# Performance work log

Measured on AMD Instinct MI355X. Metric: run time of the kernel, lower is better.

The kernel has to match this reference:

```python
import jax, jax.numpy as jnp
import numpy as np

N_FFT = 512
HOP = 160
N_ITER = 32
PAD = N_FFT // 2
TWO_PI = 2.0 * np.pi


def _stft(x, window):
    # x: [B, L] real -> spec [B, T, F] complex, center=True reflect pad (torch.stft)
    xp = jnp.pad(x, ((0, 0), (PAD, PAD)), mode='reflect')
    T = 1 + (xp.shape[-1] - N_FFT) // HOP
    idx = jnp.arange(T)[:, None] * HOP + jnp.arange(N_FFT)[None, :]  # [T, n_fft]
    frames = xp[:, idx] * window  # [B, T, n_fft]
    return jnp.fft.rfft(frames, axis=-1)  # [B, T, F]


def _istft(spec, window):
    # spec: [B, T, F] complex -> waveform [B, (T-1)*HOP] (torch.istft, center=True, length=None)
    frames = jnp.fft.irfft(spec, n=N_FFT, axis=-1) * window  # [B, T, n_fft]
    B, T, _ = frames.shape
    out_len = N_FFT + HOP * (T - 1)
    idx = (jnp.arange(T)[:, None] * HOP + jnp.arange(N_FFT)[None, :]).reshape(-1)
    y = jnp.zeros((B, out_len), frames.dtype).at[:, idx].add(frames.reshape(B, -1))
    wsq = jnp.zeros((out_len,), window.dtype).at[idx].add(jnp.tile(window * window, T))
    y = y / jnp.where(wsq > 1e-11, wsq, 1.0)  # NOLA normalization
    return y[:, PAD:out_len - PAD]


def setup_inputs() -> dict:
    key = jax.random.key(0)
    k1, k2 = jax.random.split(key)
    magnitude = jax.random.uniform(k1, (32, 1024, 257), dtype=jnp.float32)
    angles_init = jax.random.normal(k2, (32, 1024, 257), dtype=jnp.float32) * TWO_PI
    # hann window, periodic (torch.hann_window default)
    window = (0.5 * (1.0 - jnp.cos(TWO_PI * jnp.arange(N_FFT) / N_FFT))).astype(jnp.float32)
    return {"magnitude": magnitude, "angles_init": angles_init, "window": window}


def reference(magnitude, angles_init, window):
    # magnitude: [B, T, F]. Internally we keep [B, T, F] layout (torch transposes to
    # [B, F, T] before stft/istft; the math is identical, only the layout differs).
    mag = magnitude

    def step(angles, _):
        spec = mag * (jnp.cos(angles) + 1j * jnp.sin(angles))  # mag * exp(i*angles)
        wav = _istft(spec, window)
        rec = _stft(wav, window)
        new_angles = jnp.arctan2(rec.imag, rec.real)  # torch.angle
        return new_angles, None

    angles, _ = jax.lax.scan(step, angles_init, None, length=N_ITER)
    final_spec = mag * (jnp.cos(angles) + 1j * jnp.sin(angles))
    return _istft(final_spec, window)  # [B, (T-1)*HOP] = [32, 163680]
```

## Files before the change

kernel.cpp:

```cpp
#include <hip/hip_runtime.h>
#include <math.h>

#define BATCH 32
#define TFRAMES 1024
#define NBINS 257
#define NFFT 512
#define HOP 160
#define LOUT 163680
#define XPLEN 164192
#define NITER 32
#define FPW 4
#define WSTRIDE (FPW*HOP)
#define BSTRIDE (2*WSTRIDE)
#define HALO (NFFT-HOP)
#define WSPAN (WSTRIDE+HALO)
#define SPAN (BSTRIDE+HALO)
#define NBLK 128
#define SLOT SPAN
#define SB ((size_t)NBLK*SLOT)
#define SBUF ((size_t)BATCH*SB)

#define P2(i) ((i) + ((i) >> 4))

__device__ __forceinline__ float cosr(float x){ return __builtin_amdgcn_cosf(x); }
__device__ __forceinline__ float sinr(float x){ return __builtin_amdgcn_sinf(x); }
__device__ __forceinline__ void wsync(){
    __builtin_amdgcn_fence(__ATOMIC_SEQ_CST, "wavefront");
    __builtin_amdgcn_wave_barrier();
}
__device__ __forceinline__ float bperm(int addr, float v){
    return __int_as_float(__builtin_amdgcn_ds_bpermute(addr, __float_as_int(v)));
}

struct Tw { float c1,s1,c2,s2,c3,s3; };
__device__ __forceinline__ Tw twset(float x){
    Tw t; float c=cosr(x), s=sinr(x);
    t.c1=c; t.s1=s;
    t.c2=c*c-s*s; t.s2=2.f*c*s;
    t.c3=t.c2*c-t.s2*s; t.s3=t.c2*s+t.s2*c;
    return t;
}

template<int SIGN, bool TWID>
__device__ __forceinline__ void bfly4(const float xr[4], const float xi[4],
                                      const Tw& t, float yr[4], float yi[4]){
    constexpr float SG = (SIGN>0)?1.f:-1.f;
    float apc_r=xr[0]+xr[2], apc_i=xi[0]+xi[2];
    float amc_r=xr[0]-xr[2], amc_i=xi[0]-xi[2];
    float bpd_r=xr[1]+xr[3], bpd_i=xi[1]+xi[3];
    float bmd_r=xr[1]-xr[3], bmd_i=xi[1]-xi[3];
    yr[0]=apc_r+bpd_r; yi[0]=apc_i+bpd_i;
    float u2r=apc_r-bpd_r, u2i=apc_i-bpd_i;
    float u1r=amc_r-SG*bmd_i, u1i=amc_i+SG*bmd_r;
    float u3r=amc_r+SG*bmd_i, u3i=amc_i-SG*bmd_r;
    if (TWID){
        float s1=SG*t.s1, s2=SG*t.s2, s3=SG*t.s3;
        yr[1]=t.c1*u1r-s1*u1i; yi[1]=t.c1*u1i+s1*u1r;
        yr[2]=t.c2*u2r-s2*u2i; yi[2]=t.c2*u2i+s2*u2r;
        yr[3]=t.c3*u3r-s3*u3i; yi[3]=t.c3*u3i+s3*u3r;
    } else {
        yr[1]=u1r; yi[1]=u1i; yr[2]=u2r; yi[2]=u2i; yr[3]=u3r; yi[3]=u3i;
    }
}

template<int SIGN>
__device__ __forceinline__ void fft256reg(float xr[4], float xi[4],
                                          float2* __restrict__ bz,
                                          const Tw& tw0, const Tw& tw1, const Tw& tw2,
                                          int lane){
    float yr[4], yi[4], ar[4], ai[4];
    bfly4<SIGN,true>(xr, xi, tw0, yr, yi);
    { int o = 4*lane;
#pragma unroll
      for (int c=0;c<4;++c) bz[P2(o+c)] = make_float2(yr[c], yi[c]); }
    wsync();
#pragma unroll
    for (int c=0;c<4;++c){ float2 v = bz[P2(lane+64*c)]; ar[c]=v.x; ai[c]=v.y; }
    wsync();
    bfly4<SIGN,true>(ar, ai, tw1, yr, yi);
    { int o = (lane&3) + 16*(lane>>2);
#pragma unroll
      for (int c=0;c<4;++c) bz[P2(o+4*c)] = make_float2(yr[c], yi[c]); }
    wsync();
#pragma unroll
    for (int c=0;c<4;++c){ float2 v = bz[P2(lane+64*c)]; ar[c]=v.x; ai[c]=v.y; }
    wsync();
    bfly4<SIGN,true>(ar, ai, tw2, yr, yi);
    { int o = (lane&15) + 64*(lane>>4);
#pragma unroll
      for (int c=0;c<4;++c) bz[P2(o+16*c)] = make_float2(yr[c], yi[c]); }
    wsync();
#pragma unroll
    for (int c=0;c<4;++c){ float2 v = bz[P2(lane+64*c)]; ar[c]=v.x; ai[c]=v.y; }
    wsync();
    bfly4<SIGN,false>(ar, ai, tw0, xr, xi);
}

__global__ __launch_bounds__(256) void k_init(const float* __restrict__ win,
                                              float* __restrict__ wsqi){
    int i = blockIdx.x*256 + threadIdx.x;
    if (i < XPLEN){
        int n = i;
        int tmax = n / HOP; if (tmax > TFRAMES-1) tmax = TFRAMES-1;
        int tmin = (n - (NFFT-1) + (HOP-1)) / HOP; if (tmin < 0) tmin = 0;
        float acc = 0.f;
        for (int t = tmin; t <= tmax; ++t){ float w = win[n - t*HOP]; acc += w*w; }
        wsqi[i] = 1.0f / (acc > 1e-11f ? acc : 1.0f);
    }
}

__device__ __forceinline__ float xs(const float* __restrict__ Sb,
                                    const float* __restrict__ wsq, int p){
    int bxp = p / BSTRIDE, r = p - bxp*BSTRIDE;
    float a = 0.f;
    if (bxp < NBLK) a = Sb[(size_t)bxp*SLOT + r];
    if (r < HALO && bxp > 0) a += Sb[(size_t)(bxp-1)*SLOT + BSTRIDE + r];
    return a * wsq[p];
}
__device__ __forceinline__ float2 xs2(const float* __restrict__ Sb,
                                      const float* __restrict__ wsq, int p){
    int bxp = p / BSTRIDE, r = p - bxp*BSTRIDE;
    float2 acc = make_float2(0.f, 0.f);
    if (bxp < NBLK) acc = *(const float2*)(Sb + (size_t)bxp*SLOT + r);
    if (r < HALO && bxp > 0){
        float2 h = *(const float2*)(Sb + (size_t)(bxp-1)*SLOT + BSTRIDE + r);
        acc.x += h.x; acc.y += h.y;
    }
    float2 q = *(const float2*)(wsq + p);
    return make_float2(acc.x*q.x, acc.y*q.y);
}

__device__ __forceinline__ void inv_accum(float pr[4], float pi[4],
                                          float2* __restrict__ bz,
                                          const Tw& tw0, const Tw& tw1, const Tw& tw2,
                                          const float wA[4], const float wB[4],
                                          int lane, int f, float2* sa2){
    fft256reg<+1>(pr, pi, bz, tw0, tw1, tw2, lane);
    constexpr float SC = 1.f/256.f;
    int base2 = f*(HOP/2);
#pragma unroll
    for (int c=0;c<4;++c){
        int u = base2 + lane + 64*c;
        float2 v = sa2[u];
        v.x += pr[c]*wA[c]*SC;
        v.y += pi[c]*wB[c]*SC;
        sa2[u] = v;
    }
    wsync();
}

__device__ __forceinline__ void slot_store(float* __restrict__ Sw, int b, int bx,
                                           const float* s0, const float* s1, int tid){
    float2* slot2 = (float2*)(Sw + ((size_t)b*NBLK + bx)*SLOT);
    const float2* s0_2 = (const float2*)s0;
    const float2* s1_2 = (const float2*)s1;
#pragma unroll
    for (int j=0;j<7;++j){
        int u = tid + 128*j;
        if (u < SPAN/2){
            float2 v = make_float2(0.f, 0.f);
            if (u < WSPAN/2) v = s0_2[u];
            if (u >= WSTRIDE/2){
                float2 w1 = s1_2[u - WSTRIDE/2];
                v.x += w1.x; v.y += w1.y;
            }
            slot2[u] = v;
        }
    }
}

__device__ __forceinline__ void load_frame(const float* __restrict__ Sb,
                                           const float* __restrict__ wsq,
                                           int t, int lane,
                                           const float wA[4], const float wB[4],
                                           float fr[4], float fi[4]){
    bool edge = (t < 2) | (t >= TFRAMES-2);
    if (!edge){
        int pb = t*HOP;
#pragma unroll
        for (int c=0;c<4;++c){
            int p = pb + 2*(lane + 64*c);
            float2 v = xs2(Sb, wsq, p);
            fr[c] = v.x*wA[c];
            fi[c] = v.y*wB[c];
        }
    } else {
#pragma unroll
        for (int c=0;c<4;++c){
            int m = lane + 64*c;
            int p0 = t*HOP + 2*m, p1 = p0+1;
            int n0 = (p0<256)?(512-p0):((p0>=LOUT+256)?(2*LOUT+510-p0):p0);
            int n1 = (p1<256)?(512-p1):((p1>=LOUT+256)?(2*LOUT+510-p1):p1);
            fr[c] = xs(Sb, wsq, n0)*wA[c];
            fi[c] = xs(Sb, wsq, n1)*wB[c];
        }
    }
}

__device__ __forceinline__ void spectral(const float fr[4], const float fi[4],
                                         const float yr[4], const float yi[4],
                                         const float* __restrict__ magp,
                                         const float twc[4], const float tws[4],
                                         int lane, float pr[4], float pi[4]){
#pragma unroll
    for (int c=0;c<4;++c){
        int k = lane + 64*c;
        float zr = fr[c], zi = fi[c];
        float Xer = 0.5f*(zr+yr[c]), Xei = 0.5f*(zi-yi[c]);
        float Dr = zr-yr[c], Di = zi+yi[c];
        float Xor = 0.5f*Di, Xoi = -0.5f*Dr;
        float Or = twc[c]*Xor + tws[c]*Xoi;
        float Oi = twc[c]*Xoi - tws[c]*Xor;
        float X1r = Xer + Or, X1i = Xei + Oi;
        float X2r = Xer - Or, X2i = Oi - Xei;
        float q1 = X1r*X1r + X1i*X1i;
        bool ok1 = q1 > 1e-30f;
        float v1 = ok1 ? __builtin_amdgcn_rsqf(q1) : 0.f;
        float c1 = ok1 ? X1r*v1 : 1.f, s1 = X1i*v1;
        float q2 = X2r*X2r + X2i*X2i;
        bool ok2 = q2 > 1e-30f;
        float v2 = ok2 ? __builtin_amdgcn_rsqf(q2) : 0.f;
        float c2 = ok2 ? X2r*v2 : 1.f, s2 = X2i*v2;
        float m1 = magp[k], m2 = magp[256-k];
        float S1r = m1*c1, S1i = m1*s1;
        float S2r = m2*c2, S2i = m2*s2;
        float Aer = 0.5f*(S1r+S2r), Aei = 0.5f*(S1i-S2i);
        float Er = S1r - S2r, Ei = S1i + S2i;
        float Bor = 0.5f*(twc[c]*Er - tws[c]*Ei);
        float Boi = 0.5f*(twc[c]*Ei + tws[c]*Er);
        pr[c] = Aer - Boi;
        pi[c] = Aei + Bor;
    }
}

__global__ __launch_bounds__(128,4) void k_gl(const float* __restrict__ Sr,
                                              float* __restrict__ Sw,
                                              const float* __restrict__ mag,
                                              const float* __restrict__ win,
                                              const float* __restrict__ wsq){
    __shared__ __align__(16) float sacc[2][WSPAN];
    __shared__ __align__(16) float2 BZ[2][274];
    int tid = threadIdx.x, w = tid>>6, lane = tid&63;
    int b = blockIdx.y, bx = blockIdx.x;

    float2* bz = BZ[w];
    float2* sa2 = (float2*)sacc[w];

    Tw tw0 = twset((float)lane * (1.f/256.f));
    Tw tw1 = twset((float)(lane>>2) * (1.f/64.f));
    Tw tw2 = twset((float)(lane>>4) * (1.f/16.f));
    float twc[4], tws[4], wA[4], wB[4];
#pragma unroll
    for (int c=0;c<4;++c){
        int k = lane + 64*c;
        float x = (float)k * (1.f/512.f);
        twc[c]=cosr(x); tws[c]=sinr(x);
        float2 wv = ((const float2*)win)[k];
        wA[c]=wv.x; wB[c]=wv.y;
    }
    int am = ((64 - lane) & 63) << 2;
    bool l0 = (lane == 0);
#pragma unroll
    for (int j=0;j<8;++j){ int u = lane + 64*j; if (u < WSPAN/2) sa2[u]=make_float2(0.f,0.f); }
    __syncthreads();

    const float* Sb = Sr + (size_t)b*SB;
    const float* magb = mag + ((size_t)b*TFRAMES)*NBINS;
    int t0 = (bx*2 + w)*FPW;

#pragma unroll 1
    for (int f=0; f<FPW; ++f){
        int t = t0 + f;
        float fr[4], fi[4];
        load_frame(Sb, wsq, t, lane, wA, wB, fr, fi);

        fft256reg<-1>(fr, fi, bz, tw0, tw1, tw2, lane);

        float yr[4], yi[4];
#pragma unroll
        for (int c=0;c<4;++c){
            float gr = bperm(am, fr[3-c]);
            float gi = bperm(am, fi[3-c]);
            yr[c] = l0 ? fr[(4-c)&3] : gr;
            yi[c] = l0 ? fi[(4-c)&3] : gi;
        }

        float pr[4], pi[4];
        spectral(fr, fi, yr, yi, magb + (size_t)t*NBINS, twc, tws, lane, pr, pi);

        inv_accum(pr, pi, bz, tw0, tw1, tw2, wA, wB, lane, f, sa2);
    }
    __syncthreads();
    slot_store(Sw, b, bx, sacc[0], sacc[1], tid);
}

__global__ __launch_bounds__(128,4) void k_inv0s(const float* __restrict__ mag,
                                                 const float* __restrict__ ang,
                                                 const float* __restrict__ win,
                                                 float* __restrict__ Sw){
    __shared__ __align__(16) float sacc[2][WSPAN];
    __shared__ __align__(16) float2 BZ[2][274];
    int tid = threadIdx.x, w = tid>>6, lane = tid&63;
    int b = blockIdx.y, bx = blockIdx.x;

    float2* bz = BZ[w];
    float2* sa2 = (float2*)sacc[w];

    Tw tw0 = twset((float)lane * (1.f/256.f));
    Tw tw1 = twset((float)(lane>>2) * (1.f/64.f));
    Tw tw2 = twset((float)(lane>>4) * (1.f/16.f));
    float twc[4], tws[4], wA[4], wB[4];
#pragma unroll
    for (int c=0;c<4;++c){
        int k = lane + 64*c;
        float x = (float)k * (1.f/512.f);
        twc[c]=cosr(x); tws[c]=sinr(x);
        float2 wv = ((const float2*)win)[k];
        wA[c]=wv.x; wB[c]=wv.y;
    }
#pragma unroll
    for (int j=0;j<8;++j){ int u = lane + 64*j; if (u < WSPAN/2) sa2[u]=make_float2(0.f,0.f); }
    __syncthreads();

    const float* magb = mag + ((size_t)b*TFRAMES)*NBINS;
    const float* angb = ang + ((size_t)b*TFRAMES)*NBINS;
    int t0 = (bx*2 + w)*FPW;

#pragma unroll 1
    for (int f=0; f<FPW; ++f){
        int t = t0 + f;
        const float* magp = magb + (size_t)t*NBINS;
        const float* angp = angb + (size_t)t*NBINS;
        float sr_[4], si_[4];
#pragma unroll
        for (int c=0;c<4;++c){
            int k = lane + 64*c;
            float m = magp[k], a = angp[k];
            float sn, cs;
            sincosf(a, &sn, &cs);
            sr_[c] = m*cs;
            si_[c] = (c==0 && lane==0) ? 0.f : m*sn;
        }
#pragma unroll
        for (int c=0;c<4;++c){ int k=lane+64*c; bz[P2(k)] = make_float2(sr_[c], si_[c]); }
        if (lane==0){
            bz[P2(256)] = make_float2(magp[256]*cosf(angp[256]), 0.f);
        }
        wsync();
        float pr[4], pi[4];
#pragma unroll
        for (int c=0;c<4;++c){
            int k = lane + 64*c;
            float2 yv = bz[P2(256-k)];
            float Aer = 0.5f*(sr_[c]+yv.x), Aei = 0.5f*(si_[c]-yv.y);
            float Er = sr_[c]-yv.x, Ei = si_[c]+yv.y;
            float Bor = 0.5f*(twc[c]*Er - tws[c]*Ei);
            float Boi = 0.5f*(twc[c]*Ei + tws[c]*Er);
            pr[c] = Aer - Boi;
            pi[c] = Aei + Bor;
        }
        wsync();
        inv_accum(pr, pi, bz, tw0, tw1, tw2, wA, wB, lane, f, sa2);
    }
    __syncthreads();
    slot_store(Sw, b, bx, sacc[0], sacc[1], tid);
}

__global__ __launch_bounds__(128) void k_out(const float* __restrict__ S,
                                             const float* __restrict__ wsq,
                                             float* __restrict__ out){
    int b = blockIdx.y;
    int idx = blockIdx.x*128 + threadIdx.x;
    if (idx >= LOUT/2) return;
    const float* Sb = S + (size_t)b*SB;
    float2 v = xs2(Sb, wsq, 256 + 2*idx);
    ((float2*)(out + (size_t)b*LOUT))[idx] = v;
}

extern "C" void kernel_launch(void* const* d_in, const int* in_sizes, int n_in,
                              void* d_out, int out_size, void* d_ws, size_t ws_size,
                              hipStream_t stream) {
    const float* mag  = (const float*)d_in[0];
    const float* ang0 = (const float*)d_in[1];
    const float* win  = (const float*)d_in[2];
    float* ws = (float*)d_ws;
    float* S[2] = { ws, ws + SBUF };
    float* wsqi = ws + 2*SBUF;
    float* outp = (float*)d_out;

    k_init<<<(XPLEN + 255)/256, 256, 0, stream>>>(win, wsqi);

    dim3 g(NBLK, BATCH);
    k_inv0s<<<g, 128, 0, stream>>>(mag, ang0, win, S[0]);
    for (int it = 0; it < NITER; ++it){
        k_gl<<<g, 128, 0, stream>>>(S[it%2], S[(it+1)%2], mag, win, wsqi);
    }
    k_out<<<dim3(640, BATCH), 128, 0, stream>>>(S[NITER%2], wsqi, outp);
}
```

Before: 1.433 ms.

## Restructure 256-point FFT as 16x16 with 16 lanes per frame

Each 256-point complex FFT now runs on a 16-lane group, one frame per group and four frames per wave, with 16 points held in registers per lane. It uses an in-register radix-16 pass plus one XOR-swizzled LDS transpose, replacing four radix-4 stages that each needed an LDS exchange. Per-frame windowed outputs are staged in shared memory and overlap-added at block end rather than through per-wave accumulators. This cuts LDS round trips and wave syncs per FFT, but raises register pressure (occupancy hint lowered from 4 to 3) and computes twiddles with per-element sin/cos.

```diff
diff --git a/kernel.cpp b/kernel.cpp
--- a/kernel.cpp
+++ b/kernel.cpp
@@ -4,23 +4,18 @@
 #define BATCH 32
 #define TFRAMES 1024
 #define NBINS 257
-#define NFFT 512
 #define HOP 160
 #define LOUT 163680
 #define XPLEN 164192
 #define NITER 32
-#define FPW 4
-#define WSTRIDE (FPW*HOP)
-#define BSTRIDE (2*WSTRIDE)
-#define HALO (NFFT-HOP)
-#define WSPAN (WSTRIDE+HALO)
+#define BSTRIDE 1280
+#define HALO 352
 #define SPAN (BSTRIDE+HALO)
 #define NBLK 128
 #define SLOT SPAN
 #define SB ((size_t)NBLK*SLOT)
 #define SBUF ((size_t)BATCH*SB)
-
-#define P2(i) ((i) + ((i) >> 4))
+#define GSTRIDE 264
 
 __device__ __forceinline__ float cosr(float x){ return __builtin_amdgcn_cosf(x); }
 __device__ __forceinline__ float sinr(float x){ return __builtin_amdgcn_sinf(x); }
@@ -32,68 +27,86 @@
     return __int_as_float(__builtin_amdgcn_ds_bpermute(addr, __float_as_int(v)));
 }
 
-struct Tw { float c1,s1,c2,s2,c3,s3; };
-__device__ __forceinline__ Tw twset(float x){
-    Tw t; float c=cosr(x), s=sinr(x);
-    t.c1=c; t.s1=s;
-    t.c2=c*c-s*s; t.s2=2.f*c*s;
-    t.c3=t.c2*c-t.s2*s; t.s3=t.c2*s+t.s2*c;
-    return t;
-}
-
-template<int SIGN, bool TWID>
-__device__ __forceinline__ void bfly4(const float xr[4], const float xi[4],
-                                      const Tw& t, float yr[4], float yi[4]){
+template<int SIGN>
+__device__ __forceinline__ void bfly4n(const float xr[4], const float xi[4],
+                                       float yr[4], float yi[4]){
     constexpr float SG = (SIGN>0)?1.f:-1.f;
     float apc_r=xr[0]+xr[2], apc_i=xi[0]+xi[2];
     float amc_r=xr[0]-xr[2], amc_i=xi[0]-xi[2];
     float bpd_r=xr[1]+xr[3], bpd_i=xi[1]+xi[3];
     float bmd_r=xr[1]-xr[3], bmd_i=xi[1]-xi[3];
     yr[0]=apc_r+bpd_r; yi[0]=apc_i+bpd_i;
-    float u2r=apc_r-bpd_r, u2i=apc_i-bpd_i;
-    float u1r=amc_r-SG*bmd_i, u1i=amc_i+SG*bmd_r;
-    float u3r=amc_r+SG*bmd_i, u3i=amc_i-SG*bmd_r;
-    if (TWID){
-        float s1=SG*t.s1, s2=SG*t.s2, s3=SG*t.s3;
-        yr[1]=t.c1*u1r-s1*u1i; yi[1]=t.c1*u1i+s1*u1r;
-        yr[2]=t.c2*u2r-s2*u2i; yi[2]=t.c2*u2i+s2*u2r;
-        yr[3]=t.c3*u3r-s3*u3i; yi[3]=t.c3*u3i+s3*u3r;
-    } else {
-        yr[1]=u1r; yi[1]=u1i; yr[2]=u2r; yi[2]=u2i; yr[3]=u3r; yi[3]=u3i;
-    }
+    yr[2]=apc_r-bpd_r; yi[2]=apc_i-bpd_i;
+    yr[1]=amc_r-SG*bmd_i; yi[1]=amc_i+SG*bmd_r;
+    yr[3]=amc_r+SG*bmd_i; yi[3]=amc_i-SG*bmd_r;
 }
 
 template<int SIGN>
-__device__ __forceinline__ void fft256reg(float xr[4], float xi[4],
-                                          float2* __restrict__ bz,
-                                          const Tw& tw0, const Tw& tw1, const Tw& tw2,
-                                          int lane){
-    float yr[4], yi[4], ar[4], ai[4];
-    bfly4<SIGN,true>(xr, xi, tw0, yr, yi);
-    { int o = 4*lane;
-#pragma unroll
-      for (int c=0;c<4;++c) bz[P2(o+c)] = make_float2(yr[c], yi[c]); }
+__device__ __forceinline__ void fft16(float zr[16], float zi[16]){
+    constexpr float SG = (SIGN>0)?1.f:-1.f;
+    constexpr float CT16[16] = { 1.f, 0.9238795325f, 0.7071067812f, 0.3826834324f,
+                                 0.f,-0.3826834324f,-0.7071067812f,-0.9238795325f,
+                                -1.f,-0.9238795325f,-0.7071067812f,-0.3826834324f,
+                                 0.f, 0.3826834324f, 0.7071067812f, 0.9238795325f};
+    constexpr float ST16[16] = { 0.f, 0.3826834324f, 0.7071067812f, 0.9238795325f,
+                                 1.f, 0.9238795325f, 0.7071067812f, 0.3826834324f,
+                                 0.f,-0.3826834324f,-0.7071067812f,-0.9238795325f,
+                                -1.f,-0.9238795325f,-0.7071067812f,-0.3826834324f};
+    float ur[16], ui[16];
+#pragma unroll
+    for (int bq=0;bq<4;++bq){
+        float xr4[4]={zr[bq],zr[bq+4],zr[bq+8],zr[bq+12]};
+        float xi4[4]={zi[bq],zi[bq+4],zi[bq+8],zi[bq+12]};
+        float yr4[4], yi4[4];
+        bfly4n<SIGN>(xr4,xi4,yr4,yi4);
+#pragma unroll
+        for (int c=0;c<4;++c){
+            float vr=yr4[c], vi=yi4[c];
+            int J = (bq*c)&15;
+            if (J==4){ float tv=vr; vr=-SG*vi; vi=SG*tv; }
+            else if (J!=0){
+                float tr2 = CT16[J]*vr - SG*ST16[J]*vi;
+                vi        = CT16[J]*vi + SG*ST16[J]*vr;
+                vr = tr2;
+            }
+            ur[4*c+bq]=vr; ui[4*c+bq]=vi;
+        }
+    }
+#pragma unroll
+    for (int c=0;c<4;++c){
+        float xr4[4]={ur[4*c],ur[4*c+1],ur[4*c+2],ur[4*c+3]};
+        float xi4[4]={ui[4*c],ui[4*c+1],ui[4*c+2],ui[4*c+3]};
+        float yr4[4], yi4[4];
+        bfly4n<SIGN>(xr4,xi4,yr4,yi4);
+#pragma unroll
+        for (int d=0;d<4;++d){ zr[c+4*d]=yr4[d]; zi[c+4*d]=yi4[d]; }
+    }
+}
+
+template<int SIGN>
+__device__ __forceinline__ void fft256_16(float zr[16], float zi[16],
+                                          float2* __restrict__ tb, int k1l){
+    constexpr float SG = (SIGN>0)?1.f:-1.f;
+    fft16<SIGN>(zr, zi);
+    float k1f = (float)k1l;
+#pragma unroll
+    for (int r=1;r<16;++r){
+        float aa = k1f * ((float)r * (1.0f/256.0f));
+        float tc = cosr(aa), ts = SG*sinr(aa);
+        float tr2 = tc*zr[r] - ts*zi[r];
+        zi[r]     = tc*zi[r] + ts*zr[r];
+        zr[r] = tr2;
+    }
+#pragma unroll
+    for (int r=0;r<16;++r) tb[16*r + (k1l ^ r)] = make_float2(zr[r], zi[r]);
     wsync();
-#pragma unroll
-    for (int c=0;c<4;++c){ float2 v = bz[P2(lane+64*c)]; ar[c]=v.x; ai[c]=v.y; }
+    float tr[16], ti[16];
+#pragma unroll
+    for (int c=0;c<16;++c){ float2 v = tb[16*k1l + (c ^ k1l)]; tr[c]=v.x; ti[c]=v.y; }
     wsync();
-    bfly4<SIGN,true>(ar, ai, tw1, yr, yi);
-    { int o = (lane&3) + 16*(lane>>2);
-#pragma unroll
-      for (int c=0;c<4;++c) bz[P2(o+4*c)] = make_float2(yr[c], yi[c]); }
-    wsync();
-#pragma unroll
-    for (int c=0;c<4;++c){ float2 v = bz[P2(lane+64*c)]; ar[c]=v.x; ai[c]=v.y; }
-    wsync();
-    bfly4<SIGN,true>(ar, ai, tw2, yr, yi);
-    { int o = (lane&15) + 64*(lane>>4);
-#pragma unroll
-      for (int c=0;c<4;++c) bz[P2(o+16*c)] = make_float2(yr[c], yi[c]); }
-    wsync();
-#pragma unroll
-    for (int c=0;c<4;++c){ float2 v = bz[P2(lane+64*c)]; ar[c]=v.x; ai[c]=v.y; }
-    wsync();
-    bfly4<SIGN,false>(ar, ai, tw0, xr, xi);
+    fft16<SIGN>(tr, ti);
+#pragma unroll
+    for (int c=0;c<16;++c){ zr[c]=tr[c]; zi[c]=ti[c]; }
 }
 
 __global__ __launch_bounds__(256) void k_init(const float* __restrict__ win,
@@ -102,7 +115,7 @@
     if (i < XPLEN){
         int n = i;
         int tmax = n / HOP; if (tmax > TFRAMES-1) tmax = TFRAMES-1;
-        int tmin = (n - (NFFT-1) + (HOP-1)) / HOP; if (tmin < 0) tmin = 0;
+        int tmin = (n - 511 + (HOP-1)) / HOP; if (tmin < 0) tmin = 0;
         float acc = 0.f;
         for (int t = tmin; t <= tmax; ++t){ float w = win[n - t*HOP]; acc += w*w; }
         wsqi[i] = 1.0f / (acc > 1e-11f ? acc : 1.0f);
@@ -130,87 +143,106 @@
     return make_float2(acc.x*q.x, acc.y*q.y);
 }
 
-__device__ __forceinline__ void inv_accum(float pr[4], float pi[4],
-                                          float2* __restrict__ bz,
-                                          const Tw& tw0, const Tw& tw1, const Tw& tw2,
-                                          const float wA[4], const float wB[4],
-                                          int lane, int f, float2* sa2){
-    fft256reg<+1>(pr, pi, bz, tw0, tw1, tw2, lane);
+__device__ __forceinline__ void tail_store(const float zr[16], const float zi[16],
+                                           const float2* WL, float2* tb,
+                                           const float2* XB,
+                                           float* __restrict__ Sw,
+                                           int b, int bx, int tid, int k1l){
     constexpr float SC = 1.f/256.f;
-    int base2 = f*(HOP/2);
-#pragma unroll
-    for (int c=0;c<4;++c){
-        int u = base2 + lane + 64*c;
-        float2 v = sa2[u];
-        v.x += pr[c]*wA[c]*SC;
-        v.y += pi[c]*wB[c]*SC;
-        sa2[u] = v;
-    }
-    wsync();
-}
-
-__device__ __forceinline__ void slot_store(float* __restrict__ Sw, int b, int bx,
-                                           const float* s0, const float* s1, int tid){
+#pragma unroll
+    for (int c=0;c<16;++c){
+        int m = k1l + 16*c;
+        float2 wv = WL[m];
+        tb[m] = make_float2(zr[c]*wv.x*SC, zi[c]*wv.y*SC);
+    }
+    __syncthreads();
     float2* slot2 = (float2*)(Sw + ((size_t)b*NBLK + bx)*SLOT);
-    const float2* s0_2 = (const float2*)s0;
-    const float2* s1_2 = (const float2*)s1;
 #pragma unroll
     for (int j=0;j<7;++j){
         int u = tid + 128*j;
         if (u < SPAN/2){
-            float2 v = make_float2(0.f, 0.f);
-            if (u < WSPAN/2) v = s0_2[u];
-            if (u >= WSTRIDE/2){
-                float2 w1 = s1_2[u - WSTRIDE/2];
-                v.x += w1.x; v.y += w1.y;
+            float2 acc = make_float2(0.f, 0.f);
+            int f1 = u/80;            if (f1 > 7) f1 = 7;
+            int f0 = (u - 176)/80;    if (f0 < 0) f0 = 0;
+            for (int f = f0; f <= f1; ++f){
+                float2 v = XB[f*GSTRIDE + (u - 80*f)];
+                acc.x += v.x; acc.y += v.y;
             }
-            slot2[u] = v;
+            slot2[u] = acc;
         }
     }
 }
 
-__device__ __forceinline__ void load_frame(const float* __restrict__ Sb,
-                                           const float* __restrict__ wsq,
-                                           int t, int lane,
-                                           const float wA[4], const float wB[4],
-                                           float fr[4], float fi[4]){
+__global__ __launch_bounds__(128,3) void k_gl(const float* __restrict__ Sr,
+                                              float* __restrict__ Sw,
+                                              const float* __restrict__ mag,
+                                              const float* __restrict__ win,
+                                              const float* __restrict__ wsq){
+    __shared__ __align__(16) float2 XB[8*GSTRIDE];
+    __shared__ __align__(16) float2 WL[256];
+    int tid = threadIdx.x, w = tid>>6, lane = tid&63;
+    int g = lane>>4, k1l = lane&15;
+    int b = blockIdx.y, bx = blockIdx.x;
+
+    WL[tid]     = ((const float2*)win)[tid];
+    WL[tid+128] = ((const float2*)win)[tid+128];
+    __syncthreads();
+
+    int fidx = 4*w + g;
+    int t = bx*8 + fidx;
+    float2* tb = XB + fidx*GSTRIDE;
+    const float* Sb   = Sr  + (size_t)b*SB;
+    const float* magp = mag + ((size_t)b*TFRAMES + (size_t)t)*NBINS;
+
+    float zr[16], zi[16];
     bool edge = (t < 2) | (t >= TFRAMES-2);
     if (!edge){
         int pb = t*HOP;
 #pragma unroll
-        for (int c=0;c<4;++c){
-            int p = pb + 2*(lane + 64*c);
-            float2 v = xs2(Sb, wsq, p);
-            fr[c] = v.x*wA[c];
-            fi[c] = v.y*wB[c];
+        for (int r=0;r<16;++r){
+            int m = 16*r + k1l;
+            float2 v = xs2(Sb, wsq, pb + 2*m);
+            float2 wv = WL[m];
+            zr[r] = v.x*wv.x; zi[r] = v.y*wv.y;
         }
     } else {
 #pragma unroll
-        for (int c=0;c<4;++c){
-            int m = lane + 64*c;
+        for (int r=0;r<16;++r){
+            int m = 16*r + k1l;
             int p0 = t*HOP + 2*m, p1 = p0+1;
             int n0 = (p0<256)?(512-p0):((p0>=LOUT+256)?(2*LOUT+510-p0):p0);
             int n1 = (p1<256)?(512-p1):((p1>=LOUT+256)?(2*LOUT+510-p1):p1);
-            fr[c] = xs(Sb, wsq, n0)*wA[c];
-            fi[c] = xs(Sb, wsq, n1)*wB[c];
+            float2 wv = WL[m];
+            zr[r] = xs(Sb, wsq, n0)*wv.x;
+            zi[r] = xs(Sb, wsq, n1)*wv.y;
         }
     }
-}
-
-__device__ __forceinline__ void spectral(const float fr[4], const float fi[4],
-                                         const float yr[4], const float yi[4],
-                                         const float* __restrict__ magp,
-                                         const float twc[4], const float tws[4],
-                                         int lane, float pr[4], float pi[4]){
-#pragma unroll
-    for (int c=0;c<4;++c){
-        int k = lane + 64*c;
-        float zr = fr[c], zi = fi[c];
-        float Xer = 0.5f*(zr+yr[c]), Xei = 0.5f*(zi-yi[c]);
-        float Dr = zr-yr[c], Di = zi+yi[c];
+
+    fft256_16<-1>(zr, zi, tb, k1l);
+
+    int pl = (lane & 48) | ((16 - k1l) & 15);
+    int am = pl << 2;
+    bool l0 = (k1l == 0);
+    float yr[16], yi[16];
+#pragma unroll
+    for (int c=0;c<16;++c){
+        float gr = bperm(am, zr[15-c]);
+        float gi = bperm(am, zi[15-c]);
+        yr[c] = l0 ? zr[(16-c)&15] : gr;
+        yi[c] = l0 ? zi[(16-c)&15] : gi;
+    }
+
+    float a0 = (float)k1l * (1.0f/512.0f);
+#pragma unroll
+    for (int c=0;c<16;++c){
+        float aa = a0 + (float)c*(1.0f/32.0f);
+        float tc = cosr(aa), ts = sinr(aa);
+        float zrr = zr[c], zii = zi[c];
+        float Xer = 0.5f*(zrr+yr[c]), Xei = 0.5f*(zii-yi[c]);
+        float Dr = zrr-yr[c], Di = zii+yi[c];
         float Xor = 0.5f*Di, Xoi = -0.5f*Dr;
-        float Or = twc[c]*Xor + tws[c]*Xoi;
-        float Oi = twc[c]*Xoi - tws[c]*Xor;
+        float Or = tc*Xor + ts*Xoi;
+        float Oi = tc*Xoi - ts*Xor;
         float X1r = Xer + Or, X1i = Xei + Oi;
         float X2r = Xer - Or, X2i = Oi - Xei;
         float q1 = X1r*X1r + X1i*X1i;
@@ -221,149 +253,87 @@
         bool ok2 = q2 > 1e-30f;
         float v2 = ok2 ? __builtin_amdgcn_rsqf(q2) : 0.f;
         float c2 = ok2 ? X2r*v2 : 1.f, s2 = X2i*v2;
+        int k = k1l + 16*c;
         float m1 = magp[k], m2 = magp[256-k];
         float S1r = m1*c1, S1i = m1*s1;
         float S2r = m2*c2, S2i = m2*s2;
         float Aer = 0.5f*(S1r+S2r), Aei = 0.5f*(S1i-S2i);
         float Er = S1r - S2r, Ei = S1i + S2i;
-        float Bor = 0.5f*(twc[c]*Er - tws[c]*Ei);
-        float Boi = 0.5f*(twc[c]*Ei + tws[c]*Er);
-        pr[c] = Aer - Boi;
-        pi[c] = Aei + Bor;
-    }
-}
-
-__global__ __launch_bounds__(128,4) void k_gl(const float* __restrict__ Sr,
-                                              float* __restrict__ Sw,
-                                              const float* __restrict__ mag,
-                                              const float* __restrict__ win,
-                                              const float* __restrict__ wsq){
-    __shared__ __align__(16) float sacc[2][WSPAN];
-    __shared__ __align__(16) float2 BZ[2][274];
-    int tid = threadIdx.x, w = tid>>6, lane = tid&63;
-    int b = blockIdx.y, bx = blockIdx.x;
-
-    float2* bz = BZ[w];
-    float2* sa2 = (float2*)sacc[w];
-
-    Tw tw0 = twset((float)lane * (1.f/256.f));
-    Tw tw1 = twset((float)(lane>>2) * (1.f/64.f));
-    Tw tw2 = twset((float)(lane>>4) * (1.f/16.f));
-    float twc[4], tws[4], wA[4], wB[4];
-#pragma unroll
-    for (int c=0;c<4;++c){
-        int k = lane + 64*c;
-        float x = (float)k * (1.f/512.f);
-        twc[c]=cosr(x); tws[c]=sinr(x);
-        float2 wv = ((const float2*)win)[k];
-        wA[c]=wv.x; wB[c]=wv.y;
-    }
-    int am = ((64 - lane) & 63) << 2;
-    bool l0 = (lane == 0);
-#pragma unroll
-    for (int j=0;j<8;++j){ int u = lane + 64*j; if (u < WSPAN/2) sa2[u]=make_float2(0.f,0.f); }
-    __syncthreads();
-
-    const float* Sb = Sr + (size_t)b*SB;
-    const float* magb = mag + ((size_t)b*TFRAMES)*NBINS;
-    int t0 = (bx*2 + w)*FPW;
-
-#pragma unroll 1
-    for (int f=0; f<FPW; ++f){
-        int t = t0 + f;
-        float fr[4], fi[4];
-        load_frame(Sb, wsq, t, lane, wA, wB, fr, fi);
-
-        fft256reg<-1>(fr, fi, bz, tw0, tw1, tw2, lane);
-
-        float yr[4], yi[4];
-#pragma unroll
-        for (int c=0;c<4;++c){
-            float gr = bperm(am, fr[3-c]);
-            float gi = bperm(am, fi[3-c]);
-            yr[c] = l0 ? fr[(4-c)&3] : gr;
-            yi[c] = l0 ? fi[(4-c)&3] : gi;
-        }
-
-        float pr[4], pi[4];
-        spectral(fr, fi, yr, yi, magb + (size_t)t*NBINS, twc, tws, lane, pr, pi);
-
-        inv_accum(pr, pi, bz, tw0, tw1, tw2, wA, wB, lane, f, sa2);
-    }
-    __syncthreads();
-    slot_store(Sw, b, bx, sacc[0], sacc[1], tid);
-}
-
-__global__ __launch_bounds__(128,4) void k_inv0s(const float* __restrict__ mag,
+        float Bor = 0.5f*(tc*Er - ts*Ei);
+        float Boi = 0.5f*(tc*Ei + ts*Er);
+        zr[c] = Aer - Boi;
+        zi[c] = Aei + Bor;
+    }
+
+    fft256_16<+1>(zr, zi, tb, k1l);
+
+    tail_store(zr, zi, WL, tb, XB, Sw, b, bx, tid, k1l);
+}
+
+__global__ __launch_bounds__(128,3) void k_inv0s(const float* __restrict__ mag,
                                                  const float* __restrict__ ang,
                                                  const float* __restrict__ win,
                                                  float* __restrict__ Sw){
-    __shared__ __align__(16) float sacc[2][WSPAN];
-    __shared__ __align__(16) float2 BZ[2][274];
+    __shared__ __align__(16) float2 XB[8*GSTRIDE];
+    __shared__ __align__(16) float2 WL[256];
     int tid = threadIdx.x, w = tid>>6, lane = tid&63;
+    int g = lane>>4, k1l = lane&15;
     int b = blockIdx.y, bx = blockIdx.x;
 
-    float2* bz = BZ[w];
-    float2* sa2 = (float2*)sacc[w];
-
-    Tw tw0 = twset((float)lane * (1.f/256.f));
-    Tw tw1 = twset((float)(lane>>2) * (1.f/64.f));
-    Tw tw2 = twset((float)(lane>>4) * (1.f/16.f));
-    float twc[4], tws[4], wA[4], wB[4];
-#pragma unroll
-    for (int c=0;c<4;++c){
-        int k = lane + 64*c;
-        float x = (float)k * (1.f/512.f);
-        twc[c]=cosr(x); tws[c]=sinr(x);
-        float2 wv = ((const float2*)win)[k];
-        wA[c]=wv.x; wB[c]=wv.y;
-    }
-#pragma unroll
-    for (int j=0;j<8;++j){ int u = lane + 64*j; if (u < WSPAN/2) sa2[u]=make_float2(0.f,0.f); }
+    WL[tid]     = ((const float2*)win)[tid];
+    WL[tid+128] = ((const float2*)win)[tid+128];
     __syncthreads();
 
-    const float* magb = mag + ((size_t)b*TFRAMES)*NBINS;
-    const float* angb = ang + ((size_t)b*TFRAMES)*NBINS;
-    int t0 = (bx*2 + w)*FPW;
-
-#pragma unroll 1
-    for (int f=0; f<FPW; ++f){
-        int t = t0 + f;
-        const float* magp = magb + (size_t)t*NBINS;
-        const float* angp = angb + (size_t)t*NBINS;
-        float sr_[4], si_[4];
-#pragma unroll
-        for (int c=0;c<4;++c){
-            int k = lane + 64*c;
-            float m = magp[k], a = angp[k];
-            float sn, cs;
-            sincosf(a, &sn, &cs);
-            sr_[c] = m*cs;
-            si_[c] = (c==0 && lane==0) ? 0.f : m*sn;
-        }
-#pragma unroll
-        for (int c=0;c<4;++c){ int k=lane+64*c; bz[P2(k)] = make_float2(sr_[c], si_[c]); }
-        if (lane==0){
-            bz[P2(256)] = make_float2(magp[256]*cosf(angp[256]), 0.f);
-        }
-        wsync();
-        float pr[4], pi[4];
-#pragma unroll
-        for (int c=0;c<4;++c){
-            int k = lane + 64*c;
-            float2 yv = bz[P2(256-k)];
-            float Aer = 0.5f*(sr_[c]+yv.x), Aei = 0.5f*(si_[c]-yv.y);
-            float Er = sr_[c]-yv.x, Ei = si_[c]+yv.y;
-            float Bor = 0.5f*(twc[c]*Er - tws[c]*Ei);
-            float Boi = 0.5f*(twc[c]*Ei + tws[c]*Er);
-            pr[c] = Aer - Boi;
-            pi[c] = Aei + Bor;
-        }
-        wsync();
-        inv_accum(pr, pi, bz, tw0, tw1, tw2, wA, wB, lane, f, sa2);
-    }
-    __syncthreads();
-    slot_store(Sw, b, bx, sacc[0], sacc[1], tid);
+    int fidx = 4*w + g;
+    int t = bx*8 + fidx;
+    float2* tb = XB + fidx*GSTRIDE;
+    const float* magp = mag + ((size_t)b*TFRAMES + (size_t)t)*NBINS;
+    const float* angp = ang + ((size_t)b*TFRAMES + (size_t)t)*NBINS;
+
+    int pl = (lane & 48) | ((16 - k1l) & 15);
+    int am = pl << 2;
+    bool l0 = (k1l == 0);
+
+    float zr[16], zi[16];
+#pragma unroll
+    for (int r=0;r<16;++r){
+        int k = 16*r + k1l;
+        float m = magp[k], an = angp[k];
+        float sn, cs;
+        sincosf(an, &sn, &cs);
+        zr[r] = m*cs;
+        zi[r] = ((r==0) && l0) ? 0.f : m*sn;
+    }
+    float nyr = magp[256]*cosf(angp[256]);
+
+    float yr[16], yi[16];
+#pragma unroll
+    for (int c=0;c<16;++c){
+        float gr = bperm(am, zr[15-c]);
+        float gi = bperm(am, zi[15-c]);
+        float lr = (c==0) ? nyr : zr[(16-c)&15];
+        float li = (c==0) ? 0.f : zi[(16-c)&15];
+        yr[c] = l0 ? lr : gr;
+        yi[c] = l0 ? li : gi;
+    }
+
+    float a0 = (float)k1l * (1.0f/512.0f);
+#pragma unroll
+    for (int c=0;c<16;++c){
+        float aa = a0 + (float)c*(1.0f/32.0f);
+        float tc = cosr(aa), ts = sinr(aa);
+        float sr = zr[c], si = zi[c];
+        float Aer = 0.5f*(sr + yr[c]), Aei = 0.5f*(si - yi[c]);
+        float Er = sr - yr[c], Ei = si + yi[c];
+        float Bor = 0.5f*(tc*Er - ts*Ei);
+        float Boi = 0.5f*(tc*Ei + ts*Er);
+        zr[c] = Aer - Boi;
+        zi[c] = Aei + Bor;
+    }
+
+    fft256_16<+1>(zr, zi, tb, k1l);
+
+    tail_store(zr, zi, WL, tb, XB, Sw, b, bx, tid, k1l);
 }
 
 __global__ __launch_bounds__(128) void k_out(const float* __restrict__ S,
```

New measurement: 3.354 ms. +134.1%, slower.
